# Kernel tuning notes

Hardware: AMD Instinct MI355X
Metric: run time of the kernel (lower is better)

The kernel has to match this reference:

```python
import jax, jax.numpy as jnp
import numpy as np

EPS = 1e-8  # torch F.cosine_similarity eps


def setup_inputs() -> dict:
    key = jax.random.key(0)
    k1, k2 = jax.random.split(key)
    z = jax.random.normal(k1, (32768, 2048), dtype=jnp.float32)
    expert_keys = jax.random.normal(k2, (64, 2048), dtype=jnp.float32)
    return {"z": z, "expert_keys": expert_keys}


def reference(z, expert_keys):
    # cosine similarity: (z . ek) / max(||z||*||ek||, eps)  -> [N, E]
    dots = jnp.einsum("nd,ed->ne", z, expert_keys)
    z_norm = jnp.linalg.norm(z, axis=-1)            # [N]
    e_norm = jnp.linalg.norm(expert_keys, axis=-1)  # [E]
    similarity = dots / jnp.maximum(z_norm[:, None] * e_norm[None, :], EPS)
    # softmax over experts, then weighted combination of expert keys -> [N, D]
    weighted_expert = jax.nn.softmax(similarity, axis=-1) @ expert_keys
    return similarity, weighted_expert
```

## Files before the change

kernel.cpp:

```cpp
#include <hip/hip_runtime.h>
#include <hip/hip_bf16.h>

typedef __attribute__((ext_vector_type(4))) float f32x4;
typedef __attribute__((ext_vector_type(8))) short bf16x8;

#define NROWS 32768
#define DIM   2048
#define NEXP  64
#define BKF   128
#define NCH   (DIM / BKF)

__device__ __forceinline__ short f2bf(float f) {
    __hip_bfloat16 h = __float2bfloat16(f);
    short s;
    __builtin_memcpy(&s, &h, 2);
    return s;
}

__device__ __forceinline__ void async16(const void* g, void* l) {
    __builtin_amdgcn_global_load_lds(
        (const __attribute__((address_space(1))) unsigned int*)g,
        (__attribute__((address_space(3))) unsigned int*)l, 16, 0, 0);
}

__global__ __launch_bounds__(256) void prep_experts(
    const float* __restrict__ ek,
    short* __restrict__ ekbf,
    short* __restrict__ ekT,
    float* __restrict__ enorm)
{
    const int e = blockIdx.x;
    const int t = threadIdx.x;
    const float* row = ek + e * DIM;
    float ss = 0.f;
#pragma unroll
    for (int i = 0; i < 2; ++i) {
        const int c4 = t + i * 256;
        const float4 v = ((const float4*)row)[c4];
        ss += v.x * v.x + v.y * v.y + v.z * v.z + v.w * v.w;
        short4 b;
        b.x = f2bf(v.x); b.y = f2bf(v.y); b.z = f2bf(v.z); b.w = f2bf(v.w);
        *(short4*)(ekbf + e * DIM + c4 * 4) = b;
        const int d = c4 * 4;
        ekT[(d + 0) * NEXP + e] = b.x;
        ekT[(d + 1) * NEXP + e] = b.y;
        ekT[(d + 2) * NEXP + e] = b.z;
        ekT[(d + 3) * NEXP + e] = b.w;
    }
#pragma unroll
    for (int s = 1; s < 64; s <<= 1) ss += __shfl_xor(ss, s);
    __shared__ float red[4];
    if ((t & 63) == 0) red[t >> 6] = ss;
    __syncthreads();
    if (t == 0) enorm[e] = sqrtf(red[0] + red[1] + red[2] + red[3]);
}

__global__ __launch_bounds__(256) void fused_kernel(
    const float* __restrict__ z,
    const short* __restrict__ ekbf,
    const short* __restrict__ ekT,
    const float* __restrict__ enorm,
    float* __restrict__ out_sim,
    float* __restrict__ out_wei)
{
    const int tid = threadIdx.x;
    const int w   = tid >> 6;
    const int l   = tid & 63;
    const int lr  = l & 15;
    const int lg  = l >> 4;
    const int base = blockIdx.x * 32;

    union SmemU {
        float zbuf[2][32][BKF];
        float tbuf[4][32][68];
    };
    __shared__ __align__(16) SmemU U;
    __shared__ __align__(16) short ebuf[2][64][BKF];
    __shared__ __align__(16) float simL[32][64];
    __shared__ __align__(16) short WL[32][64];

    f32x4 acc[2];
    acc[0] = f32x4{0.f, 0.f, 0.f, 0.f};
    acc[1] = f32x4{0.f, 0.f, 0.f, 0.f};
    float sqa[2] = {0.f, 0.f}, sqb[2] = {0.f, 0.f};

    auto STAGE = [&](int c_) {
        const int b_ = c_ & 1;
#pragma unroll
        for (int i = 0; i < 4; ++i) {
            const int r0 = w * 8 + i * 2;
            const int zr = r0 + (l >> 5);
            async16(z + (size_t)(base + zr) * DIM + c_ * BKF
                      + (((l & 31) ^ (zr & 7)) << 2),
                    &U.zbuf[b_][r0][0]);
        }
#pragma unroll
        for (int i = 0; i < 4; ++i) {
            const int r0 = w * 16 + i * 4;
            const int er = r0 + (l >> 4);
            async16(ekbf + (size_t)er * DIM + c_ * BKF
                         + (((l & 15) ^ (er & 7)) << 3),
                    &ebuf[b_][r0][0]);
        }
    };

    STAGE(0); STAGE(1);

    for (int c = 0; c < NCH; ++c) {
        if (c < NCH - 1) asm volatile("s_waitcnt vmcnt(8)" ::: "memory");
        else             asm volatile("s_waitcnt vmcnt(0)" ::: "memory");
        __builtin_amdgcn_s_barrier();
        __builtin_amdgcn_sched_barrier(0);
        const int b = c & 1;

#pragma unroll
        for (int kk = 0; kk < BKF / 32; ++kk) {
            const int eu = ((kk * 4 + lg) ^ (lr & 7)) << 4;
            const bf16x8 bf =
                *(const bf16x8*)((const char*)&ebuf[b][w * 16 + lr][0] + eu);
#pragma unroll
            for (int mt = 0; mt < 2; ++mt) {
                const int zr = mt * 16 + lr;
                const int u0 = ((kk * 8 + lg * 2)     ^ (lr & 7)) << 4;
                const int u1 = ((kk * 8 + lg * 2 + 1) ^ (lr & 7)) << 4;
                const float4 a0 = *(const float4*)((const char*)&U.zbuf[b][zr][0] + u0);
                const float4 a1 = *(const float4*)((const char*)&U.zbuf[b][zr][0] + u1);
                sqa[mt] = fmaf(a0.x, a0.x, sqa[mt]); sqb[mt] = fmaf(a0.y, a0.y, sqb[mt]);
                sqa[mt] = fmaf(a0.z, a0.z, sqa[mt]); sqb[mt] = fmaf(a0.w, a0.w, sqb[mt]);
                sqa[mt] = fmaf(a1.x, a1.x, sqa[mt]); sqb[mt] = fmaf(a1.y, a1.y, sqb[mt]);
                sqa[mt] = fmaf(a1.z, a1.z, sqa[mt]); sqb[mt] = fmaf(a1.w, a1.w, sqb[mt]);
                bf16x8 af;
                af[0] = f2bf(a0.x); af[1] = f2bf(a0.y); af[2] = f2bf(a0.z); af[3] = f2bf(a0.w);
                af[4] = f2bf(a1.x); af[5] = f2bf(a1.y); af[6] = f2bf(a1.z); af[7] = f2bf(a1.w);
                acc[mt] = __builtin_amdgcn_mfma_f32_16x16x32_bf16(af, bf, acc[mt], 0, 0, 0);
            }
        }
        __builtin_amdgcn_s_barrier();
        if (c + 2 < NCH) STAGE(c + 2);
    }

    const float en = enorm[w * 16 + lr];
#pragma unroll
    for (int mt = 0; mt < 2; ++mt) {
        float ss = sqa[mt] + sqb[mt];
        ss += __shfl_xor(ss, 16);
        ss += __shfl_xor(ss, 32);
        const float zn = sqrtf(ss);
#pragma unroll
        for (int j = 0; j < 4; ++j) {
            const float znj = __shfl(zn, lg * 4 + j);
            const float sv = acc[mt][j] / fmaxf(znj * en, 1e-8f);
            out_sim[(size_t)(base + mt * 16 + lg * 4 + j) * NEXP + w * 16 + lr] = sv;
            simL[mt * 16 + lg * 4 + j][w * 16 + lr] = sv;
        }
    }
    __syncthreads();

    {
        const int r  = tid >> 3;
        const int cc = tid & 7;
        const float* sp = &simL[r][cc * 8];
        const f32x4 v0 = *(const f32x4*)sp;
        const f32x4 v1 = *(const f32x4*)(sp + 4);
        float va[8] = {v0[0], v0[1], v0[2], v0[3], v1[0], v1[1], v1[2], v1[3]};
        float m = va[0];
#pragma unroll
        for (int i = 1; i < 8; ++i) m = fmaxf(m, va[i]);
        m = fmaxf(m, __shfl_xor(m, 1));
        m = fmaxf(m, __shfl_xor(m, 2));
        m = fmaxf(m, __shfl_xor(m, 4));
        float sum = 0.f;
#pragma unroll
        for (int i = 0; i < 8; ++i) { va[i] = __expf(va[i] - m); sum += va[i]; }
        sum += __shfl_xor(sum, 1);
        sum += __shfl_xor(sum, 2);
        sum += __shfl_xor(sum, 4);
        const float inv = 1.0f / sum;
        bf16x8 wv;
#pragma unroll
        for (int i = 0; i < 8; ++i) wv[i] = f2bf(va[i] * inv);
        *(bf16x8*)&WL[r][(cc ^ (r & 7)) * 8] = wv;
    }
    __syncthreads();

    bf16x8 afr[2][2];
#pragma unroll
    for (int mt = 0; mt < 2; ++mt)
#pragma unroll
        for (int ks = 0; ks < 2; ++ks) {
            const int row = mt * 16 + lr;
            const int u   = (ks * 4 + lg) ^ (row & 7);
            afr[mt][ks] = *(const bf16x8*)&WL[row][u * 8];
        }

#pragma unroll 1
    for (int g = 0; g < 8; ++g) {
        f32x4 oacc[4][2];
#pragma unroll
        for (int nt2 = 0; nt2 < 4; ++nt2) {
            const int d0 = w * 512 + g * 64 + nt2 * 16;
            const short* bp = ekT + (size_t)(d0 + lr) * NEXP + lg * 8;
            const bf16x8 b0 = *(const bf16x8*)bp;
            const bf16x8 b1 = *(const bf16x8*)(bp + 32);
#pragma unroll
            for (int mt = 0; mt < 2; ++mt) {
                f32x4 o = f32x4{0.f, 0.f, 0.f, 0.f};
                o = __builtin_amdgcn_mfma_f32_16x16x32_bf16(afr[mt][0], b0, o, 0, 0, 0);
                o = __builtin_amdgcn_mfma_f32_16x16x32_bf16(afr[mt][1], b1, o, 0, 0, 0);
                oacc[nt2][mt] = o;
            }
        }
#pragma unroll
        for (int nt2 = 0; nt2 < 4; ++nt2)
#pragma unroll
            for (int mt = 0; mt < 2; ++mt)
#pragma unroll
                for (int j = 0; j < 4; ++j)
                    U.tbuf[w][mt * 16 + lg * 4 + j][nt2 * 16 + lr] = oacc[nt2][mt][j];
#pragma unroll
        for (int i = 0; i < 8; ++i) {
            const int row  = (l >> 4) + i * 4;
            const int unit = l & 15;
            const float4 t = *(const float4*)&U.tbuf[w][row][unit * 4];
            *(float4*)&out_wei[(size_t)(base + row) * DIM + w * 512 + g * 64 + unit * 4] = t;
        }
    }
}

extern "C" void kernel_launch(void* const* d_in, const int* in_sizes, int n_in,
                              void* d_out, int out_size, void* d_ws, size_t ws_size,
                              hipStream_t stream) {
    const float* z  = (const float*)d_in[0];
    const float* ek = (const float*)d_in[1];
    float* out_sim = (float*)d_out;
    float* out_wei = out_sim + (size_t)NROWS * NEXP;

    short* ekbf  = (short*)d_ws;
    short* ekT   = ekbf + NEXP * DIM;
    float* enorm = (float*)(ekT + DIM * NEXP);

    prep_experts<<<NEXP, 256, 0, stream>>>(ek, ekbf, ekT, enorm);
    fused_kernel<<<NROWS / 32, 256, 0, stream>>>(z, ekbf, ekT, enorm, out_sim, out_wei);
}
```

Before: 130.8 us.

## Warp-specialize fused kernel: sim waves stream z while MoE waves write outputs

Splits the four waves of each block into two crews. Two waves compute the cosine-similarity GEMM over a 64-row block in two 32-row tiles. The other two waves compute softmax and the weighted-expert GEMM for the previous tile and write out_wei, so z loading and output stores overlap. The MoE waves now write output directly from MFMA registers, with no LDS transpose, which makes the stores less coalesced. Fewer blocks and half the waves doing the input GEMM could reduce memory-level parallelism, and an extra tile of pipeline drain is added.

```diff
diff --git a/kernel.cpp b/kernel.cpp
--- a/kernel.cpp
+++ b/kernel.cpp
@@ -8,7 +8,10 @@
 #define DIM   2048
 #define NEXP  64
 #define BKF   128
-#define NCH   (DIM / BKF)
+#define NCH   16
+#define NTILE 2
+#define NM    (NCH * NTILE)
+#define NITER (NM + NCH)
 
 __device__ __forceinline__ short f2bf(float f) {
     __hip_bfloat16 h = __float2bfloat16(f);
@@ -55,7 +58,7 @@
     if (t == 0) enorm[e] = sqrtf(red[0] + red[1] + red[2] + red[3]);
 }
 
-__global__ __launch_bounds__(256) void fused_kernel(
+__global__ __launch_bounds__(256) void cosmoe_ws(
     const float* __restrict__ z,
     const short* __restrict__ ekbf,
     const short* __restrict__ ekT,
@@ -68,138 +71,52 @@
     const int l   = tid & 63;
     const int lr  = l & 15;
     const int lg  = l >> 4;
-    const int base = blockIdx.x * 32;
-
-    union SmemU {
-        float zbuf[2][32][BKF];
-        float tbuf[4][32][68];
-    };
-    __shared__ __align__(16) SmemU U;
+    const int base = blockIdx.x * 64;
+    const bool simCrew = (w < 2);
+    const int ws = w;
+    const int wm = w - 2;
+
+    __shared__ __align__(16) float zbuf[2][32][BKF];
     __shared__ __align__(16) short ebuf[2][64][BKF];
     __shared__ __align__(16) float simL[32][64];
     __shared__ __align__(16) short WL[32][64];
-
-    f32x4 acc[2];
-    acc[0] = f32x4{0.f, 0.f, 0.f, 0.f};
-    acc[1] = f32x4{0.f, 0.f, 0.f, 0.f};
-    float sqa[2] = {0.f, 0.f}, sqb[2] = {0.f, 0.f};
-
-    auto STAGE = [&](int c_) {
-        const int b_ = c_ & 1;
-#pragma unroll
-        for (int i = 0; i < 4; ++i) {
-            const int r0 = w * 8 + i * 2;
+    __shared__ float znL[32];
+
+    f32x4 acc[2][2];
+#pragma unroll
+    for (int a = 0; a < 2; ++a)
+#pragma unroll
+        for (int b2 = 0; b2 < 2; ++b2) acc[a][b2] = f32x4{0.f, 0.f, 0.f, 0.f};
+    float ss0 = 0.f, ss1 = 0.f;
+    bf16x8 afr[2][2];
+
+    auto STAGE = [&](int m_) {
+        const int b_ = m_ & 1;
+        const int c_ = m_ & 15;
+        const size_t rb = (size_t)(base + (m_ >> 4) * 32);
+#pragma unroll
+        for (int i = 0; i < 8; ++i) {
+            const int r0 = ws * 16 + i * 2;
             const int zr = r0 + (l >> 5);
-            async16(z + (size_t)(base + zr) * DIM + c_ * BKF
-                      + (((l & 31) ^ (zr & 7)) << 2),
-                    &U.zbuf[b_][r0][0]);
-        }
-#pragma unroll
-        for (int i = 0; i < 4; ++i) {
-            const int r0 = w * 16 + i * 4;
+            async16(z + (rb + zr) * DIM + c_ * BKF + (((l & 31) ^ (zr & 7)) << 2),
+                    &zbuf[b_][r0][0]);
+        }
+#pragma unroll
+        for (int i = 0; i < 8; ++i) {
+            const int r0 = ws * 32 + i * 4;
             const int er = r0 + (l >> 4);
-            async16(ekbf + (size_t)er * DIM + c_ * BKF
-                         + (((l & 15) ^ (er & 7)) << 3),
+            async16(ekbf + (size_t)er * DIM + c_ * BKF + (((l & 15) ^ (er & 7)) << 3),
                     &ebuf[b_][r0][0]);
         }
     };
 
-    STAGE(0); STAGE(1);
-
-    for (int c = 0; c < NCH; ++c) {
-        if (c < NCH - 1) asm volatile("s_waitcnt vmcnt(8)" ::: "memory");
-        else             asm volatile("s_waitcnt vmcnt(0)" ::: "memory");
-        __builtin_amdgcn_s_barrier();
-        __builtin_amdgcn_sched_barrier(0);
-        const int b = c & 1;
-
-#pragma unroll
-        for (int kk = 0; kk < BKF / 32; ++kk) {
-            const int eu = ((kk * 4 + lg) ^ (lr & 7)) << 4;
-            const bf16x8 bf =
-                *(const bf16x8*)((const char*)&ebuf[b][w * 16 + lr][0] + eu);
-#pragma unroll
-            for (int mt = 0; mt < 2; ++mt) {
-                const int zr = mt * 16 + lr;
-                const int u0 = ((kk * 8 + lg * 2)     ^ (lr & 7)) << 4;
-                const int u1 = ((kk * 8 + lg * 2 + 1) ^ (lr & 7)) << 4;
-                const float4 a0 = *(const float4*)((const char*)&U.zbuf[b][zr][0] + u0);
-                const float4 a1 = *(const float4*)((const char*)&U.zbuf[b][zr][0] + u1);
-                sqa[mt] = fmaf(a0.x, a0.x, sqa[mt]); sqb[mt] = fmaf(a0.y, a0.y, sqb[mt]);
-                sqa[mt] = fmaf(a0.z, a0.z, sqa[mt]); sqb[mt] = fmaf(a0.w, a0.w, sqb[mt]);
-                sqa[mt] = fmaf(a1.x, a1.x, sqa[mt]); sqb[mt] = fmaf(a1.y, a1.y, sqb[mt]);
-                sqa[mt] = fmaf(a1.z, a1.z, sqa[mt]); sqb[mt] = fmaf(a1.w, a1.w, sqb[mt]);
-                bf16x8 af;
-                af[0] = f2bf(a0.x); af[1] = f2bf(a0.y); af[2] = f2bf(a0.z); af[3] = f2bf(a0.w);
-                af[4] = f2bf(a1.x); af[5] = f2bf(a1.y); af[6] = f2bf(a1.z); af[7] = f2bf(a1.w);
-                acc[mt] = __builtin_amdgcn_mfma_f32_16x16x32_bf16(af, bf, acc[mt], 0, 0, 0);
-            }
-        }
-        __builtin_amdgcn_s_barrier();
-        if (c + 2 < NCH) STAGE(c + 2);
-    }
-
-    const float en = enorm[w * 16 + lr];
-#pragma unroll
-    for (int mt = 0; mt < 2; ++mt) {
-        float ss = sqa[mt] + sqb[mt];
-        ss += __shfl_xor(ss, 16);
-        ss += __shfl_xor(ss, 32);
-        const float zn = sqrtf(ss);
-#pragma unroll
-        for (int j = 0; j < 4; ++j) {
-            const float znj = __shfl(zn, lg * 4 + j);
-            const float sv = acc[mt][j] / fmaxf(znj * en, 1e-8f);
-            out_sim[(size_t)(base + mt * 16 + lg * 4 + j) * NEXP + w * 16 + lr] = sv;
-            simL[mt * 16 + lg * 4 + j][w * 16 + lr] = sv;
-        }
-    }
-    __syncthreads();
-
-    {
-        const int r  = tid >> 3;
-        const int cc = tid & 7;
-        const float* sp = &simL[r][cc * 8];
-        const f32x4 v0 = *(const f32x4*)sp;
-        const f32x4 v1 = *(const f32x4*)(sp + 4);
-        float va[8] = {v0[0], v0[1], v0[2], v0[3], v1[0], v1[1], v1[2], v1[3]};
-        float m = va[0];
-#pragma unroll
-        for (int i = 1; i < 8; ++i) m = fmaxf(m, va[i]);
-        m = fmaxf(m, __shfl_xor(m, 1));
-        m = fmaxf(m, __shfl_xor(m, 2));
-        m = fmaxf(m, __shfl_xor(m, 4));
-        float sum = 0.f;
-#pragma unroll
-        for (int i = 0; i < 8; ++i) { va[i] = __expf(va[i] - m); sum += va[i]; }
-        sum += __shfl_xor(sum, 1);
-        sum += __shfl_xor(sum, 2);
-        sum += __shfl_xor(sum, 4);
-        const float inv = 1.0f / sum;
-        bf16x8 wv;
-#pragma unroll
-        for (int i = 0; i < 8; ++i) wv[i] = f2bf(va[i] * inv);
-        *(bf16x8*)&WL[r][(cc ^ (r & 7)) * 8] = wv;
-    }
-    __syncthreads();
-
-    bf16x8 afr[2][2];
-#pragma unroll
-    for (int mt = 0; mt < 2; ++mt)
-#pragma unroll
-        for (int ks = 0; ks < 2; ++ks) {
-            const int row = mt * 16 + lr;
-            const int u   = (ks * 4 + lg) ^ (row & 7);
-            afr[mt][ks] = *(const bf16x8*)&WL[row][u * 8];
-        }
-
-#pragma unroll 1
-    for (int g = 0; g < 8; ++g) {
-        f32x4 oacc[4][2];
-#pragma unroll
-        for (int nt2 = 0; nt2 < 4; ++nt2) {
-            const int d0 = w * 512 + g * 64 + nt2 * 16;
-            const short* bp = ekT + (size_t)(d0 + lr) * NEXP + lg * 8;
+    auto MOESLICE = [&](int t, int s) {
+        const int d0 = wm * 1024 + s * 32;
+        const size_t rb = (size_t)(base + t * 32);
+        f32x4 oacc[2][2];
+#pragma unroll
+        for (int nt2 = 0; nt2 < 2; ++nt2) {
+            const short* bp = ekT + (size_t)(d0 + nt2 * 16 + lr) * NEXP + lg * 8;
             const bf16x8 b0 = *(const bf16x8*)bp;
             const bf16x8 b1 = *(const bf16x8*)(bp + 32);
 #pragma unroll
@@ -211,18 +128,140 @@
             }
         }
 #pragma unroll
-        for (int nt2 = 0; nt2 < 4; ++nt2)
+        for (int nt2 = 0; nt2 < 2; ++nt2)
 #pragma unroll
             for (int mt = 0; mt < 2; ++mt)
 #pragma unroll
                 for (int j = 0; j < 4; ++j)
-                    U.tbuf[w][mt * 16 + lg * 4 + j][nt2 * 16 + lr] = oacc[nt2][mt][j];
-#pragma unroll
-        for (int i = 0; i < 8; ++i) {
-            const int row  = (l >> 4) + i * 4;
-            const int unit = l & 15;
-            const float4 t = *(const float4*)&U.tbuf[w][row][unit * 4];
-            *(float4*)&out_wei[(size_t)(base + row) * DIM + w * 512 + g * 64 + unit * 4] = t;
+                    out_wei[(rb + mt * 16 + lg * 4 + j) * DIM + d0 + nt2 * 16 + lr]
+                        = oacc[nt2][mt][j];
+    };
+
+    if (simCrew) { STAGE(0); STAGE(1); }
+
+#pragma unroll 1
+    for (int m = 0; m < NITER; ++m) {
+        const bool simAct = m < NM;
+        if (simCrew && simAct) {
+            if (m < NM - 1) asm volatile("s_waitcnt vmcnt(16)" ::: "memory");
+            else            asm volatile("s_waitcnt vmcnt(0)"  ::: "memory");
+        }
+        __builtin_amdgcn_s_barrier();
+        __builtin_amdgcn_sched_barrier(0);
+
+        if (simCrew && simAct) {
+            const int b = m & 1;
+#pragma unroll
+            for (int kk = 0; kk < 4; ++kk) {
+                bf16x8 af[2];
+#pragma unroll
+                for (int mt = 0; mt < 2; ++mt) {
+                    const char* zp = (const char*)&zbuf[b][mt * 16 + lr][0];
+                    const float4 a0 = *(const float4*)(zp + (((kk * 8 + lg * 2)     ^ (lr & 7)) << 4));
+                    const float4 a1 = *(const float4*)(zp + (((kk * 8 + lg * 2 + 1) ^ (lr & 7)) << 4));
+                    if (mt == ws) {
+                        ss0 = fmaf(a0.x, a0.x, ss0); ss1 = fmaf(a0.y, a0.y, ss1);
+                        ss0 = fmaf(a0.z, a0.z, ss0); ss1 = fmaf(a0.w, a0.w, ss1);
+                        ss0 = fmaf(a1.x, a1.x, ss0); ss1 = fmaf(a1.y, a1.y, ss1);
+                        ss0 = fmaf(a1.z, a1.z, ss0); ss1 = fmaf(a1.w, a1.w, ss1);
+                    }
+                    af[mt][0] = f2bf(a0.x); af[mt][1] = f2bf(a0.y);
+                    af[mt][2] = f2bf(a0.z); af[mt][3] = f2bf(a0.w);
+                    af[mt][4] = f2bf(a1.x); af[mt][5] = f2bf(a1.y);
+                    af[mt][6] = f2bf(a1.z); af[mt][7] = f2bf(a1.w);
+                }
+#pragma unroll
+                for (int nt = 0; nt < 2; ++nt) {
+                    const int er = ws * 32 + nt * 16 + lr;
+                    const bf16x8 bf = *(const bf16x8*)((const char*)&ebuf[b][er][0]
+                                        + (((kk * 4 + lg) ^ (lr & 7)) << 4));
+                    acc[0][nt] = __builtin_amdgcn_mfma_f32_16x16x32_bf16(af[0], bf, acc[0][nt], 0, 0, 0);
+                    acc[1][nt] = __builtin_amdgcn_mfma_f32_16x16x32_bf16(af[1], bf, acc[1][nt], 0, 0, 0);
+                }
+            }
+        }
+        if (!simCrew && m >= NCH) {
+            const int t  = (m - NCH) >> 4;
+            const int s0 = ((m - NCH) & 15) * 2;
+            MOESLICE(t, s0);
+            MOESLICE(t, s0 + 1);
+        }
+        asm volatile("s_waitcnt lgkmcnt(0)" ::: "memory");
+        __builtin_amdgcn_s_barrier();
+        if (simCrew && simAct && m + 2 < NM) STAGE(m + 2);
+
+        if (simAct && (m & 15) == 15) {
+            const int t = m >> 4;
+            if (simCrew) {
+                float ssq = ss0 + ss1;
+                ssq += __shfl_xor(ssq, 16);
+                ssq += __shfl_xor(ssq, 32);
+                if (l < 16) znL[ws * 16 + l] = sqrtf(ssq);
+#pragma unroll
+                for (int mt = 0; mt < 2; ++mt)
+#pragma unroll
+                    for (int nt = 0; nt < 2; ++nt)
+#pragma unroll
+                        for (int j = 0; j < 4; ++j)
+                            simL[mt * 16 + lg * 4 + j][ws * 32 + nt * 16 + lr] = acc[mt][nt][j];
+#pragma unroll
+                for (int a = 0; a < 2; ++a)
+#pragma unroll
+                    for (int b2 = 0; b2 < 2; ++b2) acc[a][b2] = f32x4{0.f, 0.f, 0.f, 0.f};
+                ss0 = 0.f; ss1 = 0.f;
+            }
+            asm volatile("s_waitcnt lgkmcnt(0)" ::: "memory");
+            __builtin_amdgcn_s_barrier();
+            if (!simCrew) {
+                const int local = wm * 64 + l;
+                const int r  = local >> 2;
+                const int cc = local & 3;
+                float sv[16];
+                const float zn = znL[r];
+#pragma unroll
+                for (int i = 0; i < 16; ++i) {
+                    const float en = enorm[cc * 16 + i];
+                    sv[i] = simL[r][cc * 16 + i] / fmaxf(zn * en, 1e-8f);
+                }
+                float* op = out_sim + (size_t)(base + t * 32 + r) * NEXP + cc * 16;
+#pragma unroll
+                for (int i = 0; i < 4; ++i) {
+                    float4 v;
+                    v.x = sv[i*4]; v.y = sv[i*4+1]; v.z = sv[i*4+2]; v.w = sv[i*4+3];
+                    *(float4*)(op + i * 4) = v;
+                }
+                float mx = sv[0];
+#pragma unroll
+                for (int i = 1; i < 16; ++i) mx = fmaxf(mx, sv[i]);
+                mx = fmaxf(mx, __shfl_xor(mx, 1));
+                mx = fmaxf(mx, __shfl_xor(mx, 2));
+                float sum = 0.f;
+#pragma unroll
+                for (int i = 0; i < 16; ++i) { sv[i] = __expf(sv[i] - mx); sum += sv[i]; }
+                sum += __shfl_xor(sum, 1);
+                sum += __shfl_xor(sum, 2);
+                const float inv = 1.0f / sum;
+                bf16x8 w0, w1;
+#pragma unroll
+                for (int i = 0; i < 8; ++i) {
+                    w0[i] = f2bf(sv[i] * inv);
+                    w1[i] = f2bf(sv[8 + i] * inv);
+                }
+                *(bf16x8*)&WL[r][((cc * 2)     ^ (r & 7)) * 8] = w0;
+                *(bf16x8*)&WL[r][((cc * 2 + 1) ^ (r & 7)) * 8] = w1;
+            }
+            asm volatile("s_waitcnt lgkmcnt(0)" ::: "memory");
+            __builtin_amdgcn_s_barrier();
+            if (!simCrew) {
+#pragma unroll
+                for (int mt = 0; mt < 2; ++mt)
+#pragma unroll
+                    for (int ks = 0; ks < 2; ++ks) {
+                        const int row = mt * 16 + lr;
+                        const int u   = (ks * 4 + lg) ^ (row & 7);
+                        afr[mt][ks] = *(const bf16x8*)&WL[row][u * 8];
+                    }
+            }
         }
     }
 }
@@ -240,5 +279,5 @@
     float* enorm = (float*)(ekT + DIM * NEXP);
 
     prep_experts<<<NEXP, 256, 0, stream>>>(ek, ekbf, ekT, enorm);
-    fused_kernel<<<NROWS / 32, 256, 0, stream>>>(z, ekbf, ekT, enorm, out_sim, out_wei);
-}
+    cosmoe_ws<<<NROWS / 64, 256, 0, stream>>>(z, ekbf, ekT, enorm, out_sim, out_wei);
+}
```

Result: slower. 146.2 us (+11.8%).

## Process two row tiles per block with parity-dependent phase ordering

Applied to the files above, without the earlier changes.

Each block now handles 64 rows as two 32-row tiles, and the grid is halved. Half the blocks run read-heavy similarity phases back to back and then both write-heavy output phases, so reads of z and writes of the weighted output are meant to overlap across blocks and keep both HBM directions busy. The similarity tile is no longer kept in LDS: softmax reads it back from global out_sim after a vmcnt(0) wait and a barrier. This adds a global round trip and relies on cache coherence for that readback, and fewer blocks may reduce latency hiding.

```diff
diff --git a/kernel.cpp b/kernel.cpp
--- a/kernel.cpp
+++ b/kernel.cpp
@@ -55,20 +55,22 @@
     if (t == 0) enorm[e] = sqrtf(red[0] + red[1] + red[2] + red[3]);
 }
 
-__global__ __launch_bounds__(256) void fused_kernel(
+__global__ __launch_bounds__(256) void fused2(
     const float* __restrict__ z,
     const short* __restrict__ ekbf,
     const short* __restrict__ ekT,
     const float* __restrict__ enorm,
-    float* __restrict__ out_sim,
-    float* __restrict__ out_wei)
+    float*                    out_sim,
+    float* __restrict__       out_wei)
 {
     const int tid = threadIdx.x;
     const int w   = tid >> 6;
     const int l   = tid & 63;
     const int lr  = l & 15;
     const int lg  = l >> 4;
-    const int base = blockIdx.x * 32;
+    const int bx  = blockIdx.x;
+    const int base = bx * 64;
+    const int parity = (bx ^ (bx >> 3) ^ (bx >> 8)) & 1;
 
     union SmemU {
         float zbuf[2][32][BKF];
@@ -76,93 +78,95 @@
     };
     __shared__ __align__(16) SmemU U;
     __shared__ __align__(16) short ebuf[2][64][BKF];
-    __shared__ __align__(16) float simL[32][64];
-    __shared__ __align__(16) short WL[32][64];
-
-    f32x4 acc[2];
-    acc[0] = f32x4{0.f, 0.f, 0.f, 0.f};
-    acc[1] = f32x4{0.f, 0.f, 0.f, 0.f};
-    float sqa[2] = {0.f, 0.f}, sqb[2] = {0.f, 0.f};
-
-    auto STAGE = [&](int c_) {
-        const int b_ = c_ & 1;
-#pragma unroll
-        for (int i = 0; i < 4; ++i) {
-            const int r0 = w * 8 + i * 2;
-            const int zr = r0 + (l >> 5);
-            async16(z + (size_t)(base + zr) * DIM + c_ * BKF
-                      + (((l & 31) ^ (zr & 7)) << 2),
-                    &U.zbuf[b_][r0][0]);
+    __shared__ __align__(16) short WL[2][32][64];
+
+    auto SIM_TILE = [&](int t) {
+        const int rbase = base + t * 32;
+        f32x4 acc[2];
+        acc[0] = f32x4{0.f, 0.f, 0.f, 0.f};
+        acc[1] = f32x4{0.f, 0.f, 0.f, 0.f};
+        float sqa[2] = {0.f, 0.f}, sqb[2] = {0.f, 0.f};
+
+        auto STAGE = [&](int c_) {
+            const int b_ = c_ & 1;
+#pragma unroll
+            for (int i = 0; i < 4; ++i) {
+                const int r0 = w * 8 + i * 2;
+                const int zr = r0 + (l >> 5);
+                async16(z + (size_t)(rbase + zr) * DIM + c_ * BKF
+                          + (((l & 31) ^ (zr & 7)) << 2),
+                        &U.zbuf[b_][r0][0]);
+            }
+#pragma unroll
+            for (int i = 0; i < 4; ++i) {
+                const int r0 = w * 16 + i * 4;
+                const int er = r0 + (l >> 4);
+                async16(ekbf + (size_t)er * DIM + c_ * BKF
+                             + (((l & 15) ^ (er & 7)) << 3),
+                        &ebuf[b_][r0][0]);
+            }
+        };
+
+        STAGE(0); STAGE(1);
+
+        for (int c = 0; c < NCH; ++c) {
+            if (c < NCH - 1) asm volatile("s_waitcnt vmcnt(8)" ::: "memory");
+            else             asm volatile("s_waitcnt vmcnt(0)" ::: "memory");
+            __builtin_amdgcn_s_barrier();
+            __builtin_amdgcn_sched_barrier(0);
+            const int b = c & 1;
+
+#pragma unroll
+            for (int kk = 0; kk < BKF / 32; ++kk) {
+                const int eu = ((kk * 4 + lg) ^ (lr & 7)) << 4;
+                const bf16x8 bf =
+                    *(const bf16x8*)((const char*)&ebuf[b][w * 16 + lr][0] + eu);
+#pragma unroll
+                for (int mt = 0; mt < 2; ++mt) {
+                    const int zr = mt * 16 + lr;
+                    const int u0 = ((kk * 8 + lg * 2)     ^ (lr & 7)) << 4;
+                    const int u1 = ((kk * 8 + lg * 2 + 1) ^ (lr & 7)) << 4;
+                    const float4 a0 = *(const float4*)((const char*)&U.zbuf[b][zr][0] + u0);
+                    const float4 a1 = *(const float4*)((const char*)&U.zbuf[b][zr][0] + u1);
+                    sqa[mt] = fmaf(a0.x, a0.x, sqa[mt]); sqb[mt] = fmaf(a0.y, a0.y, sqb[mt]);
+                    sqa[mt] = fmaf(a0.z, a0.z, sqa[mt]); sqb[mt] = fmaf(a0.w, a0.w, sqb[mt]);
+                    sqa[mt] = fmaf(a1.x, a1.x, sqa[mt]); sqb[mt] = fmaf(a1.y, a1.y, sqb[mt]);
+                    sqa[mt] = fmaf(a1.z, a1.z, sqa[mt]); sqb[mt] = fmaf(a1.w, a1.w, sqb[mt]);
+                    bf16x8 af;
+                    af[0] = f2bf(a0.x); af[1] = f2bf(a0.y); af[2] = f2bf(a0.z); af[3] = f2bf(a0.w);
+                    af[4] = f2bf(a1.x); af[5] = f2bf(a1.y); af[6] = f2bf(a1.z); af[7] = f2bf(a1.w);
+                    acc[mt] = __builtin_amdgcn_mfma_f32_16x16x32_bf16(af, bf, acc[mt], 0, 0, 0);
+                }
+            }
+            __builtin_amdgcn_s_barrier();
+            if (c + 2 < NCH) STAGE(c + 2);
         }
-#pragma unroll
-        for (int i = 0; i < 4; ++i) {
-            const int r0 = w * 16 + i * 4;
-            const int er = r0 + (l >> 4);
-            async16(ekbf + (size_t)er * DIM + c_ * BKF
-                         + (((l & 15) ^ (er & 7)) << 3),
-                    &ebuf[b_][r0][0]);
+
+        const float en = enorm[w * 16 + lr];
+#pragma unroll
+        for (int mt = 0; mt < 2; ++mt) {
+            float ss = sqa[mt] + sqb[mt];
+            ss += __shfl_xor(ss, 16);
+            ss += __shfl_xor(ss, 32);
+            const float zn = sqrtf(ss);
+#pragma unroll
+            for (int j = 0; j < 4; ++j) {
+                const float znj = __shfl(zn, lg * 4 + j);
+                out_sim[(size_t)(rbase + mt * 16 + lg * 4 + j) * NEXP + w * 16 + lr]
+                    = acc[mt][j] / fmaxf(znj * en, 1e-8f);
+            }
         }
-    };
-
-    STAGE(0); STAGE(1);
-
-    for (int c = 0; c < NCH; ++c) {
-        if (c < NCH - 1) asm volatile("s_waitcnt vmcnt(8)" ::: "memory");
-        else             asm volatile("s_waitcnt vmcnt(0)" ::: "memory");
+        asm volatile("s_waitcnt vmcnt(0)" ::: "memory");
         __builtin_amdgcn_s_barrier();
-        __builtin_amdgcn_sched_barrier(0);
-        const int b = c & 1;
-
-#pragma unroll
-        for (int kk = 0; kk < BKF / 32; ++kk) {
-            const int eu = ((kk * 4 + lg) ^ (lr & 7)) << 4;
-            const bf16x8 bf =
-                *(const bf16x8*)((const char*)&ebuf[b][w * 16 + lr][0] + eu);
-#pragma unroll
-            for (int mt = 0; mt < 2; ++mt) {
-                const int zr = mt * 16 + lr;
-                const int u0 = ((kk * 8 + lg * 2)     ^ (lr & 7)) << 4;
-                const int u1 = ((kk * 8 + lg * 2 + 1) ^ (lr & 7)) << 4;
-                const float4 a0 = *(const float4*)((const char*)&U.zbuf[b][zr][0] + u0);
-                const float4 a1 = *(const float4*)((const char*)&U.zbuf[b][zr][0] + u1);
-                sqa[mt] = fmaf(a0.x, a0.x, sqa[mt]); sqb[mt] = fmaf(a0.y, a0.y, sqb[mt]);
-                sqa[mt] = fmaf(a0.z, a0.z, sqa[mt]); sqb[mt] = fmaf(a0.w, a0.w, sqb[mt]);
-                sqa[mt] = fmaf(a1.x, a1.x, sqa[mt]); sqb[mt] = fmaf(a1.y, a1.y, sqb[mt]);
-                sqa[mt] = fmaf(a1.z, a1.z, sqa[mt]); sqb[mt] = fmaf(a1.w, a1.w, sqb[mt]);
-                bf16x8 af;
-                af[0] = f2bf(a0.x); af[1] = f2bf(a0.y); af[2] = f2bf(a0.z); af[3] = f2bf(a0.w);
-                af[4] = f2bf(a1.x); af[5] = f2bf(a1.y); af[6] = f2bf(a1.z); af[7] = f2bf(a1.w);
-                acc[mt] = __builtin_amdgcn_mfma_f32_16x16x32_bf16(af, bf, acc[mt], 0, 0, 0);
-            }
-        }
-        __builtin_amdgcn_s_barrier();
-        if (c + 2 < NCH) STAGE(c + 2);
-    }
-
-    const float en = enorm[w * 16 + lr];
-#pragma unroll
-    for (int mt = 0; mt < 2; ++mt) {
-        float ss = sqa[mt] + sqb[mt];
-        ss += __shfl_xor(ss, 16);
-        ss += __shfl_xor(ss, 32);
-        const float zn = sqrtf(ss);
-#pragma unroll
-        for (int j = 0; j < 4; ++j) {
-            const float znj = __shfl(zn, lg * 4 + j);
-            const float sv = acc[mt][j] / fmaxf(znj * en, 1e-8f);
-            out_sim[(size_t)(base + mt * 16 + lg * 4 + j) * NEXP + w * 16 + lr] = sv;
-            simL[mt * 16 + lg * 4 + j][w * 16 + lr] = sv;
-        }
-    }
-    __syncthreads();
-
-    {
+    };
+
+    auto SOFTMAX_TILE = [&](int t) {
         const int r  = tid >> 3;
         const int cc = tid & 7;
-        const float* sp = &simL[r][cc * 8];
-        const f32x4 v0 = *(const f32x4*)sp;
-        const f32x4 v1 = *(const f32x4*)(sp + 4);
-        float va[8] = {v0[0], v0[1], v0[2], v0[3], v1[0], v1[1], v1[2], v1[3]};
+        const float* sp = out_sim + (size_t)(base + t * 32 + r) * NEXP + cc * 8;
+        const float4 v0 = *(const float4*)sp;
+        const float4 v1 = *(const float4*)(sp + 4);
+        float va[8] = {v0.x, v0.y, v0.z, v0.w, v1.x, v1.y, v1.z, v1.w};
         float m = va[0];
 #pragma unroll
         for (int i = 1; i < 8; ++i) m = fmaxf(m, va[i]);
@@ -179,51 +183,64 @@
         bf16x8 wv;
 #pragma unroll
         for (int i = 0; i < 8; ++i) wv[i] = f2bf(va[i] * inv);
-        *(bf16x8*)&WL[r][(cc ^ (r & 7)) * 8] = wv;
-    }
-    __syncthreads();
-
-    bf16x8 afr[2][2];
-#pragma unroll
-    for (int mt = 0; mt < 2; ++mt)
-#pragma unroll
-        for (int ks = 0; ks < 2; ++ks) {
-            const int row = mt * 16 + lr;
-            const int u   = (ks * 4 + lg) ^ (row & 7);
-            afr[mt][ks] = *(const bf16x8*)&WL[row][u * 8];
+        *(bf16x8*)&WL[t][r][(cc ^ (r & 7)) * 8] = wv;
+        __syncthreads();
+    };
+
+    auto MOE_TILE = [&](int t) {
+        const int rbase = base + t * 32;
+        bf16x8 afr[2][2];
+#pragma unroll
+        for (int mt = 0; mt < 2; ++mt)
+#pragma unroll
+            for (int ks = 0; ks < 2; ++ks) {
+                const int row = mt * 16 + lr;
+                const int u   = (ks * 4 + lg) ^ (row & 7);
+                afr[mt][ks] = *(const bf16x8*)&WL[t][row][u * 8];
+            }
+
+#pragma unroll 1
+        for (int g = 0; g < 8; ++g) {
+            f32x4 oacc[4][2];
+#pragma unroll
+            for (int nt2 = 0; nt2 < 4; ++nt2) {
+                const int d0 = w * 512 + g * 64 + nt2 * 16;
+                const short* bp = ekT + (size_t)(d0 + lr) * NEXP + lg * 8;
+                const bf16x8 b0 = *(const bf16x8*)bp;
+                const bf16x8 b1 = *(const bf16x8*)(bp + 32);
+#pragma unroll
+                for (int mt = 0; mt < 2; ++mt) {
+                    f32x4 o = f32x4{0.f, 0.f, 0.f, 0.f};
+                    o = __builtin_amdgcn_mfma_f32_16x16x32_bf16(afr[mt][0], b0, o, 0, 0, 0);
+                    o = __builtin_amdgcn_mfma_f32_16x16x32_bf16(afr[mt][1], b1, o, 0, 0, 0);
+                    oacc[nt2][mt] = o;
+                }
+            }
+#pragma unroll
+            for (int nt2 = 0; nt2 < 4; ++nt2)
+#pragma unroll
+                for (int mt = 0; mt < 2; ++mt)
+#pragma unroll
+                    for (int j = 0; j < 4; ++j)
+                        U.tbuf[w][mt * 16 + lg * 4 + j][nt2 * 16 + lr] = oacc[nt2][mt][j];
+#pragma unroll
+            for (int i = 0; i < 8; ++i) {
+                const int row  = (l >> 4) + i * 4;
+                const int unit = l & 15;
+                const float4 v = *(const float4*)&U.tbuf[w][row][unit * 4];
+                *(float4*)&out_wei[(size_t)(rbase + row) * DIM + w * 512 + g * 64 + unit * 4] = v;
+            }
         }
-
-#pragma unroll 1
-    for (int g = 0; g < 8; ++g) {
-        f32x4 oacc[4][2];
-#pragma unroll
-        for (int nt2 = 0; nt2 < 4; ++nt2) {
-            const int d0 = w * 512 + g * 64 + nt2 * 16;
-            const short* bp = ekT + (size_t)(d0 + lr) * NEXP + lg * 8;
-            const bf16x8 b0 = *(const bf16x8*)bp;
-            const bf16x8 b1 = *(const bf16x8*)(bp + 32);
-#pragma unroll
-            for (int mt = 0; mt < 2; ++mt) {
-                f32x4 o = f32x4{0.f, 0.f, 0.f, 0.f};
-                o = __builtin_amdgcn_mfma_f32_16x16x32_bf16(afr[mt][0], b0, o, 0, 0, 0);
-                o = __builtin_amdgcn_mfma_f32_16x16x32_bf16(afr[mt][1], b1, o, 0, 0, 0);
-                oacc[nt2][mt] = o;
-            }
-        }
-#pragma unroll
-        for (int nt2 = 0; nt2 < 4; ++nt2)
-#pragma unroll
-            for (int mt = 0; mt < 2; ++mt)
-#pragma unroll
-                for (int j = 0; j < 4; ++j)
-                    U.tbuf[w][mt * 16 + lg * 4 + j][nt2 * 16 + lr] = oacc[nt2][mt][j];
-#pragma unroll
-        for (int i = 0; i < 8; ++i) {
-            const int row  = (l >> 4) + i * 4;
-            const int unit = l & 15;
-            const float4 t = *(const float4*)&U.tbuf[w][row][unit * 4];
-            *(float4*)&out_wei[(size_t)(base + row) * DIM + w * 512 + g * 64 + unit * 4] = t;
-        }
+        __syncthreads();
+    };
+
+    if (parity == 0) {
+        SIM_TILE(0); SOFTMAX_TILE(0); MOE_TILE(0);
+        SIM_TILE(1); SOFTMAX_TILE(1); MOE_TILE(1);
+    } else {
+        SIM_TILE(0); SOFTMAX_TILE(0);
+        SIM_TILE(1); SOFTMAX_TILE(1);
+        MOE_TILE(0); MOE_TILE(1);
     }
 }
 
@@ -240,5 +257,5 @@
     float* enorm = (float*)(ekT + DIM * NEXP);
 
     prep_experts<<<NEXP, 256, 0, stream>>>(ek, ekbf, ekT, enorm);
-    fused_kernel<<<NROWS / 32, 256, 0, stream>>>(z, ekbf, ekT, enorm, out_sim, out_wei);
-}
+    fused2<<<NROWS / 64, 256, 0, stream>>>(z, ekbf, ekT, enorm, out_sim, out_wei);
+}
```

New measurement: 156.5 us. +19.6%, slower.
